# Kernel tuning notes

Measured on AMD Instinct MI355X. Metric: run time of the kernel, lower is better.

## Reference

```python
import jax, jax.numpy as jnp
import numpy as np

D_MODEL = 1024
NUM_HEADS = 16
D_HEAD = D_MODEL // NUM_HEADS
LN_EPS = 1e-5
ROPE_BASE = 10000.0


def layer_norm(x, w, b=None, eps=LN_EPS):
    mu = jnp.mean(x, axis=-1, keepdims=True)
    var = jnp.mean(jnp.square(x - mu), axis=-1, keepdims=True)
    y = (x - mu) * jax.lax.rsqrt(var + eps) * w
    return y + b if b is not None else y


def _rotate_half(x):
    x1, x2 = jnp.split(x, 2, axis=-1)
    return jnp.concatenate([-x2, x1], axis=-1)


def apply_rotary(q, k):
    # q, k: [B, S, H, Dh]
    s, dh = q.shape[1], q.shape[-1]
    inv_freq = 1.0 / (ROPE_BASE ** (jnp.arange(0, dh, 2, dtype=jnp.float32) / dh))
    t = jnp.arange(s, dtype=jnp.float32)
    freqs = jnp.outer(t, inv_freq)                      # [S, Dh/2]
    emb = jnp.concatenate([freqs, freqs], axis=-1)      # [S, Dh]
    cos = jnp.cos(emb)[None, :, None, :].astype(q.dtype)
    sin = jnp.sin(emb)[None, :, None, :].astype(q.dtype)
    q_rot = q * cos + _rotate_half(q) * sin
    k_rot = k * cos + _rotate_half(k) * sin
    return q_rot, k_rot


def setup_inputs() -> dict:
    key = jax.random.key(0)
    ks = jax.random.split(key, 8)
    B, L, D = 4, 2048, D_MODEL
    x = jax.random.normal(ks[0], (B, L, D), dtype=jnp.float32)
    sequence_id = jnp.sort(jax.random.randint(ks[1], (B, L), 0, 8), axis=-1).astype(jnp.int64)
    scale = 1.0 / np.sqrt(D)
    return {
        "x": x,
        "sequence_id": sequence_id,
        "ln_w": jnp.ones((D,), jnp.float32),
        "ln_b": jnp.zeros((D,), jnp.float32),
        "w_qkv": jax.random.normal(ks[2], (D, 3 * D), jnp.float32) * scale,
        "q_ln_w": jnp.ones((D,), jnp.float32),
        "k_ln_w": jnp.ones((D,), jnp.float32),
        "w_out": jax.random.normal(ks[3], (D, D), jnp.float32) * scale,
    }


def reference(x, sequence_id, ln_w, ln_b, w_qkv, q_ln_w, k_ln_w, w_out):
    B, L, D = x.shape
    H, Dh = NUM_HEADS, D_HEAD
    # fused LayerNorm + QKV projection
    qkv = layer_norm(x, ln_w, ln_b) @ w_qkv              # [B, L, 3D]
    q, k, v = jnp.split(qkv, 3, axis=-1)
    # qk layernorm (scale only, bias=False)
    q = layer_norm(q, q_ln_w)
    k = layer_norm(k, k_ln_w)
    # split heads and apply rotary
    q = q.reshape(B, L, H, Dh)
    k = k.reshape(B, L, H, Dh)
    q, k = apply_rotary(q, k)
    v = v.reshape(B, L, H, Dh)
    # packed-sequence mask: tokens attend only within same sequence id
    mask = (sequence_id[:, :, None] == sequence_id[:, None, :])[:, None, :, :]  # [B,1,L,L]
    scale = 1.0 / np.sqrt(Dh)
    scores = jnp.einsum("bqhd,bkhd->bhqk", q, k) * scale
    scores = jnp.where(mask, scores, jnp.finfo(scores.dtype).min)
    attn = jax.nn.softmax(scores, axis=-1)
    ctx = jnp.einsum("bhqk,bkhd->bqhd", attn, v).reshape(B, L, D)
    return ctx @ w_out
```

## Files before the change

kernel.cpp:

```cpp
#include <hip/hip_runtime.h>
#include <hip/hip_bf16.h>
#include <cstdint>
#include <cstddef>
#include <type_traits>

#define D_MODEL 1024
#define NH      16
#define DH      64
#define LSEQ    2048
#define BATCH   4
#define NTOK    8192
#define K3      3072

typedef __attribute__((ext_vector_type(8))) short  short8;
typedef __attribute__((ext_vector_type(4))) float  floatx4;

__device__ __forceinline__ unsigned short f2bf_bits(float f) {
  __hip_bfloat16 h = __float2bfloat16(f);
  return __builtin_bit_cast(unsigned short, h);
}
__device__ __forceinline__ float bf2f(unsigned short u) {
  return __bfloat162float(__builtin_bit_cast(__hip_bfloat16, u));
}
__device__ __forceinline__ unsigned int pack_bf16(float lo, float hi) {
  return (unsigned int)f2bf_bits(lo) | ((unsigned int)f2bf_bits(hi) << 16);
}

__device__ __forceinline__ void gld_lds16(const void* g, void* l) {
  __builtin_amdgcn_global_load_lds(
      (const __attribute__((address_space(1))) void*)g,
      (__attribute__((address_space(3))) void*)l,
      16, 0, 0);
}

__global__ __launch_bounds__(256)
void prep_kernel(const float* __restrict__ x, const float* __restrict__ ln_w,
                 const float* __restrict__ ln_b, const float* __restrict__ w_qkv,
                 const float* __restrict__ w_out, const int* __restrict__ sid,
                 __hip_bfloat16* __restrict__ hbuf, __hip_bfloat16* __restrict__ wqkvT,
                 __hip_bfloat16* __restrict__ woutT, int* __restrict__ segstart,
                 int* __restrict__ segend) {
  __shared__ __align__(16) char smem[8448];
  const int blk = blockIdx.x;
  const int tid = threadIdx.x;

  if (blk < 4096) {
    float (*tile)[33] = reinterpret_cast<float(*)[33]>(smem);
    const float* src;  __hip_bfloat16* dst;  int R, C, bx, by;
    if (blk < 3072) { src = w_qkv; dst = wqkvT; R = 1024; C = 3072; bx = blk % 96; by = blk / 96; }
    else            { src = w_out; dst = woutT; R = 1024; C = 1024; bx = (blk - 3072) & 31; by = (blk - 3072) >> 5; }
    const int c0 = bx * 32, r0 = by * 32;
    const int xx = tid & 31, yy = tid >> 5;
    #pragma unroll
    for (int j = 0; j < 32; j += 8)
      tile[yy + j][xx] = src[(size_t)(r0 + yy + j) * C + c0 + xx];
    __syncthreads();
    #pragma unroll
    for (int j = 0; j < 32; j += 8)
      dst[(size_t)(c0 + yy + j) * R + r0 + xx] = __float2bfloat16(tile[xx][yy + j]);
  } else if (blk < 6144) {
    const int lane = tid & 63;
    const int t = (blk - 4096) * 4 + (tid >> 6);
    const float4* xr = reinterpret_cast<const float4*>(x) + (size_t)t * 256;
    float4 v[4];
    float s = 0.f, ss = 0.f;
    #pragma unroll
    for (int i = 0; i < 4; i++) {
      v[i] = xr[lane + i * 64];
      s  += (v[i].x + v[i].y) + (v[i].z + v[i].w);
      ss += (v[i].x*v[i].x + v[i].y*v[i].y) + (v[i].z*v[i].z + v[i].w*v[i].w);
    }
    #pragma unroll
    for (int off = 1; off < 64; off <<= 1) {
      s  += __shfl_xor(s, off);
      ss += __shfl_xor(ss, off);
    }
    const float mu = s * (1.f / 1024);
    const float rs = rsqrtf(ss * (1.f / 1024) - mu * mu + 1e-5f);
    const float4* wr = reinterpret_cast<const float4*>(ln_w);
    const float4* br = reinterpret_cast<const float4*>(ln_b);
    ushort4* hr = reinterpret_cast<ushort4*>(hbuf) + (size_t)t * 256;
    #pragma unroll
    for (int i = 0; i < 4; i++) {
      const float4 wv = wr[lane + i * 64];
      const float4 bv = br[lane + i * 64];
      ushort4 o;
      o.x = f2bf_bits((v[i].x - mu) * rs * wv.x + bv.x);
      o.y = f2bf_bits((v[i].y - mu) * rs * wv.y + bv.y);
      o.z = f2bf_bits((v[i].z - mu) * rs * wv.z + bv.z);
      o.w = f2bf_bits((v[i].w - mu) * rs * wv.w + bv.w);
      hr[lane + i * 64] = o;
    }
  } else {
    int* srow = reinterpret_cast<int*>(smem);
    const int sblk = blk - 6144;
    const int b = sblk >> 3;
    const int* row = sid + (size_t)b * LSEQ;
    #pragma unroll
    for (int i = 0; i < 8; i++) srow[tid + i * 256] = row[tid + i * 256];
    __syncthreads();
    const int l = (sblk & 7) * 256 + tid;
    const int v = srow[l];
    int lo = 0, hi = l;
    while (lo < hi) { int mid = (lo + hi) >> 1; if (srow[mid] < v) lo = mid + 1; else hi = mid; }
    const int i = b * LSEQ + l;
    segstart[i] = lo;
    lo = l + 1; hi = LSEQ;
    while (lo < hi) { int mid = (lo + hi) >> 1; if (srow[mid] <= v) lo = mid + 1; else hi = mid; }
    segend[i] = lo;
  }
}

template <typename OutT>
__global__ __launch_bounds__(256, 2)
void gemm_bt(const __hip_bfloat16* __restrict__ A, const __hip_bfloat16* __restrict__ Bt,
             OutT* __restrict__ C, int M, int N, int K) {
  const int tid  = threadIdx.x;
  const int lane = tid & 63;
  const int wave = tid >> 6;
  const int bm = blockIdx.y * 128;
  const int bn = blockIdx.x * 128;
  const int wm = (wave & 1) * 64;
  const int wn = (wave >> 1) * 64;
  const int quad = lane >> 4;
  const int l16  = lane & 15;

  __shared__ __align__(16) __hip_bfloat16 As[128 * 64];
  __shared__ __align__(16) __hip_bfloat16 Bs[128 * 64];

  floatx4 acc[4][4];
  #pragma unroll
  for (int i = 0; i < 4; i++)
    #pragma unroll
    for (int j = 0; j < 4; j++) {
      floatx4 z = {0.f, 0.f, 0.f, 0.f};
      acc[i][j] = z;
    }

  const int srow = tid >> 3;
  const int sq   = tid & 7;
  const int sc8  = (sq ^ (srow & 7)) * 8;
  const __hip_bfloat16* Ab = A  + (size_t)(bm + srow) * K + sc8;
  const __hip_bfloat16* Bb = Bt + (size_t)(bn + srow) * K + sc8;

  const int axr = l16 & 7;

  for (int k0 = 0; k0 < K; k0 += 64) {
    __syncthreads();
    #pragma unroll
    for (int p = 0; p < 4; p++) {
      gld_lds16(Ab + (size_t)(p * 32) * K + k0, (char*)As + p * 4096 + tid * 16);
      gld_lds16(Bb + (size_t)(p * 32) * K + k0, (char*)Bs + p * 4096 + tid * 16);
    }
    __syncthreads();
    #pragma unroll
    for (int s0 = 0; s0 < 2; s0++) {
      const int qo = ((s0 * 4 + quad) ^ axr) * 8;
      short8 af[4], bfr[4];
      #pragma unroll
      for (int i = 0; i < 4; i++)
        af[i] = *reinterpret_cast<const short8*>(As + (wm + i * 16 + l16) * 64 + qo);
      #pragma unroll
      for (int j = 0; j < 4; j++)
        bfr[j] = *reinterpret_cast<const short8*>(Bs + (wn + j * 16 + l16) * 64 + qo);
      #pragma unroll
      for (int i = 0; i < 4; i++)
        #pragma unroll
        for (int j = 0; j < 4; j++)
          acc[i][j] = __builtin_amdgcn_mfma_f32_16x16x32_bf16(af[i], bfr[j], acc[i][j], 0, 0, 0);
    }
  }

  #pragma unroll
  for (int i = 0; i < 4; i++)
    #pragma unroll
    for (int j = 0; j < 4; j++) {
      const int row0 = bm + wm + i * 16 + quad * 4;
      const int col  = bn + wn + j * 16 + l16;
      #pragma unroll
      for (int r = 0; r < 4; r++) {
        if constexpr (std::is_same<OutT, __hip_bfloat16>::value)
          C[(size_t)(row0 + r) * N + col] = __float2bfloat16(acc[i][j][r]);
        else
          C[(size_t)(row0 + r) * N + col] = acc[i][j][r];
      }
    }
}

__global__ __launch_bounds__(256)
void ropevt_kernel(const unsigned short* __restrict__ qkv, const float* __restrict__ qw,
                   const float* __restrict__ kw, unsigned short* __restrict__ qT,
                   unsigned short* __restrict__ kT, unsigned short* __restrict__ vT) {
  __shared__ __align__(16) unsigned short T[64 * 64];
  const int blk = blockIdx.x;
  const int tid = threadIdx.x;

  if (blk < 2048) {
    const int lane = tid & 63;
    const int t = blk * 4 + (tid >> 6);
    const int b = t >> 11, l = t & 2047;
    const unsigned short* row = qkv + (size_t)t * K3;
    const int hh = lane >> 2;
    const int jb = (lane & 3) * 8;
    const int base = hh * 64 + jb;

    const short8 qa_u = *reinterpret_cast<const short8*>(row + base);
    const short8 qb_u = *reinterpret_cast<const short8*>(row + base + 32);
    const short8 ka_u = *reinterpret_cast<const short8*>(row + 1024 + base);
    const short8 kb_u = *reinterpret_cast<const short8*>(row + 1024 + base + 32);

    float qa[8], qb[8], ka[8], kb[8];
    float s_q = 0.f, ss_q = 0.f, s_k = 0.f, ss_k = 0.f;
    #pragma unroll
    for (int e = 0; e < 8; e++) {
      qa[e] = bf2f((unsigned short)qa_u[e]); qb[e] = bf2f((unsigned short)qb_u[e]);
      ka[e] = bf2f((unsigned short)ka_u[e]); kb[e] = bf2f((unsigned short)kb_u[e]);
      s_q  += qa[e] + qb[e];  ss_q += qa[e]*qa[e] + qb[e]*qb[e];
      s_k  += ka[e] + kb[e];  ss_k += ka[e]*ka[e] + kb[e]*kb[e];
    }
    #pragma unroll
    for (int off = 1; off < 64; off <<= 1) {
      s_q  += __shfl_xor(s_q, off);  ss_q += __shfl_xor(ss_q, off);
      s_k  += __shfl_xor(s_k, off);  ss_k += __shfl_xor(ss_k, off);
    }
    const float qmu = s_q * (1.f/1024);
    const float qrs = rsqrtf(ss_q * (1.f/1024) - qmu*qmu + 1e-5f);
    const float kmu = s_k * (1.f/1024);
    const float krs = rsqrtf(ss_k * (1.f/1024) - kmu*kmu + 1e-5f);

    const int j0 = lane & 31;
    const float invf = __expf(-(float)j0 * 0.28782313662425575f);
    float tsin, tcos;
    sincosf((float)l * invf, &tsin, &tcos);

    const float4 wq0 = *reinterpret_cast<const float4*>(qw + base);
    const float4 wq1 = *reinterpret_cast<const float4*>(qw + base + 4);
    const float4 wq2 = *reinterpret_cast<const float4*>(qw + base + 32);
    const float4 wq3 = *reinterpret_cast<const float4*>(qw + base + 36);
    const float4 wk0 = *reinterpret_cast<const float4*>(kw + base);
    const float4 wk1 = *reinterpret_cast<const float4*>(kw + base + 4);
    const float4 wk2 = *reinterpret_cast<const float4*>(kw + base + 32);
    const float4 wk3 = *reinterpret_cast<const float4*>(kw + base + 36);
    const float wqa[8] = {wq0.x,wq0.y,wq0.z,wq0.w, wq1.x,wq1.y,wq1.z,wq1.w};
    const float wqb[8] = {wq2.x,wq2.y,wq2.z,wq2.w, wq3.x,wq3.y,wq3.z,wq3.w};
    const float wka[8] = {wk0.x,wk0.y,wk0.z,wk0.w, wk1.x,wk1.y,wk1.z,wk1.w};
    const float wkb[8] = {wk2.x,wk2.y,wk2.z,wk2.w, wk3.x,wk3.y,wk3.z,wk3.w};

    short8 oqa, oqb, oka, okb;
    #pragma unroll
    for (int e = 0; e < 8; e++) {
      const int j = jb + e;
      const float c  = __shfl(tcos, j);
      const float sn = __shfl(tsin, j);
      const float qn1 = (qa[e] - qmu) * qrs * wqa[e];
      const float qn2 = (qb[e] - qmu) * qrs * wqb[e];
      const float kn1 = (ka[e] - kmu) * krs * wka[e];
      const float kn2 = (kb[e] - kmu) * krs * wkb[e];
      oqa[e] = (short)f2bf_bits((qn1 * c - qn2 * sn) * 0.125f);
      oqb[e] = (short)f2bf_bits((qn2 * c + qn1 * sn) * 0.125f);
      oka[e] = (short)f2bf_bits(kn1 * c - kn2 * sn);
      okb[e] = (short)f2bf_bits(kn2 * c + kn1 * sn);
    }
    const size_t ob = ((size_t)(b * NH + hh) * LSEQ + l) * DH + jb;
    *reinterpret_cast<short8*>(qT + ob)      = oqa;
    *reinterpret_cast<short8*>(qT + ob + 32) = oqb;
    *reinterpret_cast<short8*>(kT + ob)      = oka;
    *reinterpret_cast<short8*>(kT + ob + 32) = okb;
  } else {
    const int blkv = blk - 2048;
    const int l0 = (blkv & 31) * 64;
    const int bh = blkv >> 5;
    const int b = bh >> 4, h = bh & 15;
    const int sr = tid >> 3, scc = tid & 7;
    const int r1 = sr + 32;
    gld_lds16(qkv + (size_t)(b * LSEQ + l0 + sr) * K3 + 2048 + h * 64 + ((scc ^ ((sr >> 3) & 7)) * 8),
              (char*)T + tid * 16);
    gld_lds16(qkv + (size_t)(b * LSEQ + l0 + r1) * K3 + 2048 + h * 64 + ((scc ^ ((r1 >> 3) & 7)) * 8),
              (char*)T + 4096 + tid * 16);
    __syncthreads();
    #pragma unroll
    for (int it = 0; it < 2; it++) {
      const int cid = tid + it * 256;
      const int dh = cid >> 3, c = (cid & 7) * 8;
      const int sl = (dh >> 3) ^ ((c >> 3) & 7);
      short8 o;
      #pragma unroll
      for (int e = 0; e < 8; e++)
        o[e] = (short)T[(c + e) * 64 + sl * 8 + (dh & 7)];
      *reinterpret_cast<short8*>(vT + ((size_t)bh * DH + dh) * LSEQ + l0 + c) = o;
    }
  }
}

__global__ __launch_bounds__(256, 2)
void attn_mfma(const unsigned short* __restrict__ qT, const unsigned short* __restrict__ kT,
               const unsigned short* __restrict__ vT, const int* __restrict__ segs,
               const int* __restrict__ sege, unsigned short* __restrict__ ctx) {
  const int tid  = threadIdx.x;
  const int lane = tid & 63, w = tid >> 6;
  const int quad = lane >> 4, l16 = lane & 15;

  const int fid = blockIdx.x + (blockIdx.y << 4) + (blockIdx.z << 8);
  const int sw  = (fid & 7) * 128 + (fid >> 3);
  const int qbase = (sw & 15) * 128;
  const int h = (sw >> 4) & 15, b = sw >> 8;

  const size_t bh = (size_t)(b * NH + h);
  const unsigned short* Kg = kT + bh * LSEQ * DH;
  const unsigned short* Vg = vT + bh * DH * LSEQ;

  __shared__ __align__(16) unsigned short Ps[4][32 * 72];

  short8 qf[2][2];
  int st[2], en[2], gmin[2], gmax[2];
  #pragma unroll
  for (int g = 0; g < 2; g++) {
    const int qy = qbase + w * 32 + g * 16 + l16;
    const unsigned short* Qrow = qT + (bh * LSEQ + qy) * DH;
    qf[g][0] = *reinterpret_cast<const short8*>(Qrow + quad * 8);
    qf[g][1] = *reinterpret_cast<const short8*>(Qrow + 32 + quad * 8);
    st[g] = segs[b * LSEQ + qy];
    en[g] = sege[b * LSEQ + qy];
    gmin[g] = segs[b * LSEQ + qbase + w * 32 + g * 16];
    gmax[g] = sege[b * LSEQ + qbase + w * 32 + g * 16 + 15];
  }
  const int wstart = gmin[0] & ~63;
  const int wmax   = gmax[1];

  floatx4 acc[2][4];
  #pragma unroll
  for (int g = 0; g < 2; g++)
    #pragma unroll
    for (int dt = 0; dt < 4; dt++) { floatx4 z = {0.f,0.f,0.f,0.f}; acc[g][dt] = z; }
  float m[2] = {9.f, 9.f};
  float lsum[2] = {0.f, 0.f};

  short8 kf[4][2];
  #pragma unroll
  for (int t = 0; t < 4; t++) {
    const unsigned short* kp = Kg + (size_t)(wstart + t * 16 + l16) * DH + quad * 8;
    kf[t][0] = *reinterpret_cast<const short8*>(kp);
    kf[t][1] = *reinterpret_cast<const short8*>(kp + 32);
  }

  for (int kk = wstart; kk < wmax; kk += 64) {
    const bool have_next = (kk + 64) < wmax;

    short8 vf[4][2];
    #pragma unroll
    for (int dt = 0; dt < 4; dt++) {
      const unsigned short* vp = Vg + (size_t)(dt * 16 + l16) * LSEQ + kk + quad * 8;
      vf[dt][0] = *reinterpret_cast<const short8*>(vp);
      vf[dt][1] = *reinterpret_cast<const short8*>(vp + 32);
    }
    short8 kn[4][2];
    if (have_next) {
      #pragma unroll
      for (int t = 0; t < 4; t++) {
        const unsigned short* kp = Kg + (size_t)(kk + 64 + t * 16 + l16) * DH + quad * 8;
        kn[t][0] = *reinterpret_cast<const short8*>(kp);
        kn[t][1] = *reinterpret_cast<const short8*>(kp + 32);
      }
    }

    bool act[2];
    #pragma unroll
    for (int g = 0; g < 2; g++)
      act[g] = !(kk + 64 <= gmin[g] || kk >= gmax[g]);

    #pragma unroll
    for (int g = 0; g < 2; g++) {
      if (!act[g]) continue;

      floatx4 sc[4];
      __builtin_amdgcn_s_setprio(1);
      #pragma unroll
      for (int t = 0; t < 4; t++) {
        floatx4 z = {0.f,0.f,0.f,0.f};
        sc[t] = __builtin_amdgcn_mfma_f32_16x16x32_bf16(kf[t][0], qf[g][0], z, 0, 0, 0);
        sc[t] = __builtin_amdgcn_mfma_f32_16x16x32_bf16(kf[t][1], qf[g][1], sc[t], 0, 0, 0);
      }
      __builtin_amdgcn_s_setprio(0);

      const unsigned span = (unsigned)(en[g] - st[g]);
      float vm = -1e30f;
      #pragma unroll
      for (int t = 0; t < 4; t++) {
        const int k0 = kk + t * 16 + quad * 4;
        #pragma unroll
        for (int r = 0; r < 4; r++) {
          const bool ok = (unsigned)(k0 + r - st[g]) < span;
          sc[t][r] = ok ? sc[t][r] : -1e30f;
          vm = fmaxf(vm, sc[t][r]);
        }
      }

      if (__any(vm > m[g])) {
        float vv = fmaxf(vm, __shfl_xor(vm, 16));
        vv = fmaxf(vv, __shfl_xor(vv, 32));
        const float a = __expf(m[g] - vv);
        lsum[g] *= a;
        #pragma unroll
        for (int dt = 0; dt < 4; dt++)
          #pragma unroll
          for (int r = 0; r < 4; r++) acc[g][dt][r] *= a;
        m[g] = vv;
      }

      const float mn = m[g];
      float rs = 0.f;
      #pragma unroll
      for (int t = 0; t < 4; t++) {
        const float p0 = __expf(sc[t][0] - mn);
        const float p1 = __expf(sc[t][1] - mn);
        const float p2 = __expf(sc[t][2] - mn);
        const float p3 = __expf(sc[t][3] - mn);
        rs += (p0 + p1) + (p2 + p3);
        uint2 pk;
        pk.x = pack_bf16(p0, p1);
        pk.y = pack_bf16(p2, p3);
        *reinterpret_cast<uint2*>(&Ps[w][(g * 16 + l16) * 72 + t * 16 + quad * 4]) = pk;
      }
      lsum[g] += rs;
    }

    short8 pf[2][2];
    #pragma unroll
    for (int g = 0; g < 2; g++) {
      if (!act[g]) continue;
      pf[g][0] = *reinterpret_cast<const short8*>(&Ps[w][(g * 16 + l16) * 72 + quad * 8]);
      pf[g][1] = *reinterpret_cast<const short8*>(&Ps[w][(g * 16 + l16) * 72 + 32 + quad * 8]);
    }
    __builtin_amdgcn_s_setprio(1);
    #pragma unroll
    for (int dt = 0; dt < 4; dt++) {
      #pragma unroll
      for (int g = 0; g < 2; g++) {
        if (!act[g]) continue;
        acc[g][dt] = __builtin_amdgcn_mfma_f32_16x16x32_bf16(vf[dt][0], pf[g][0], acc[g][dt], 0, 0, 0);
        acc[g][dt] = __builtin_amdgcn_mfma_f32_16x16x32_bf16(vf[dt][1], pf[g][1], acc[g][dt], 0, 0, 0);
      }
    }
    __builtin_amdgcn_s_setprio(0);

    if (have_next) {
      #pragma unroll
      for (int t = 0; t < 4; t++) {
        kf[t][0] = kn[t][0];
        kf[t][1] = kn[t][1];
      }
    }
  }

  #pragma unroll
  for (int g = 0; g < 2; g++) {
    lsum[g] += __shfl_xor(lsum[g], 16);
    lsum[g] += __shfl_xor(lsum[g], 32);
    const float inv = (lsum[g] > 0.f) ? 1.f / lsum[g] : 0.f;
    const int qy = qbase + w * 32 + g * 16 + l16;
    unsigned short* orow = ctx + ((size_t)(b * LSEQ + qy)) * D_MODEL + h * DH;
    #pragma unroll
    for (int dt = 0; dt < 4; dt++) {
      uint2 o;
      o.x = pack_bf16(acc[g][dt][0] * inv, acc[g][dt][1] * inv);
      o.y = pack_bf16(acc[g][dt][2] * inv, acc[g][dt][3] * inv);
      *reinterpret_cast<uint2*>(orow + dt * 16 + quad * 4) = o;
    }
  }
}

extern "C" void kernel_launch(void* const* d_in, const int* in_sizes, int n_in,
                              void* d_out, int out_size, void* d_ws, size_t ws_size,
                              hipStream_t stream) {
  const float* x      = (const float*)d_in[0];
  const int*   sid    = (const int*)d_in[1];
  const float* ln_w   = (const float*)d_in[2];
  const float* ln_b   = (const float*)d_in[3];
  const float* w_qkv  = (const float*)d_in[4];
  const float* q_ln_w = (const float*)d_in[5];
  const float* k_ln_w = (const float*)d_in[6];
  const float* w_out  = (const float*)d_in[7];
  float* out = (float*)d_out;
  char* ws = (char*)d_ws;

  constexpr size_t OFF_WQKVT = 0;
  constexpr size_t OFF_WOUTT = 6291456;
  constexpr size_t OFF_H     = 8388608;
  constexpr size_t OFF_QKV   = 25165824;
  constexpr size_t OFF_QT    = 75497472;
  constexpr size_t OFF_KT    = 92274688;
  constexpr size_t OFF_VT    = 109051904;
  constexpr size_t OFF_CTX   = 125829120;
  constexpr size_t OFF_SEGS  = 142606336;
  constexpr size_t OFF_SEGE  = 142639104;

  __hip_bfloat16* wqkvT = (__hip_bfloat16*)(ws + OFF_WQKVT);
  __hip_bfloat16* woutT = (__hip_bfloat16*)(ws + OFF_WOUTT);
  __hip_bfloat16* hbuf  = (__hip_bfloat16*)(ws + OFF_H);
  __hip_bfloat16* qkvb  = (__hip_bfloat16*)(ws + OFF_QKV);
  unsigned short* qTb   = (unsigned short*)(ws + OFF_QT);
  unsigned short* kTb   = (unsigned short*)(ws + OFF_KT);
  unsigned short* vTb   = (unsigned short*)(ws + OFF_VT);
  unsigned short* ctx   = (unsigned short*)(ws + OFF_CTX);
  int*            segst = (int*)(ws + OFF_SEGS);
  int*            segen = (int*)(ws + OFF_SEGE);

  prep_kernel<<<6176, 256, 0, stream>>>(x, ln_w, ln_b, w_qkv, w_out, sid,
                                        hbuf, wqkvT, woutT, segst, segen);
  gemm_bt<__hip_bfloat16><<<dim3(K3 / 128, NTOK / 128), 256, 0, stream>>>(
      hbuf, wqkvT, qkvb, NTOK, K3, 1024);
  ropevt_kernel<<<4096, 256, 0, stream>>>((const unsigned short*)qkvb, q_ln_w, k_ln_w,
                                          qTb, kTb, vTb);
  attn_mfma<<<dim3(LSEQ / 128, NH, BATCH), 256, 0, stream>>>(qTb, kTb, vTb, segst, segen, ctx);
  gemm_bt<float><<<dim3(D_MODEL / 128, NTOK / 128), 256, 0, stream>>>(
      (const __hip_bfloat16*)ctx, woutT, out, NTOK, D_MODEL, 1024);
}
```

Before: 254.6 us.

## Split attention key range across wave pairs and merge partial softmax in LDS

The attention kernel now launches 512 threads per block. Each pair of waves shares the same 32 queries and splits the key blocks between them by alternating 64-key chunks. The two partial results (accumulators, running max and sum) are merged through shared memory using a flash-decoding style rescale. This is meant to shorten each wave's serial key loop and raise parallelism, since the packed-sequence mask gives only a few key blocks per query. In exchange it adds an extra LDS buffer, a block-wide barrier, and merge arithmetic, and it drops the block-index swizzle.

```diff
diff --git a/kernel.cpp b/kernel.cpp
--- a/kernel.cpp
+++ b/kernel.cpp
@@ -292,39 +292,40 @@
   }
 }
 
-__global__ __launch_bounds__(256, 2)
+__global__ __launch_bounds__(512, 4)
 void attn_mfma(const unsigned short* __restrict__ qT, const unsigned short* __restrict__ kT,
                const unsigned short* __restrict__ vT, const int* __restrict__ segs,
                const int* __restrict__ sege, unsigned short* __restrict__ ctx) {
   const int tid  = threadIdx.x;
   const int lane = tid & 63, w = tid >> 6;
+  const int pair = w >> 1, half = w & 1;
   const int quad = lane >> 4, l16 = lane & 15;
 
-  const int fid = blockIdx.x + (blockIdx.y << 4) + (blockIdx.z << 8);
-  const int sw  = (fid & 7) * 128 + (fid >> 3);
-  const int qbase = (sw & 15) * 128;
-  const int h = (sw >> 4) & 15, b = sw >> 8;
-
+  const int qbase = blockIdx.x * 128;
+  const int h = blockIdx.y, b = blockIdx.z;
   const size_t bh = (size_t)(b * NH + h);
   const unsigned short* Kg = kT + bh * LSEQ * DH;
   const unsigned short* Vg = vT + bh * DH * LSEQ;
 
-  __shared__ __align__(16) unsigned short Ps[4][32 * 72];
+  __shared__ __align__(16) unsigned short Ps[8][32 * 72];
+  __shared__ __align__(16) float MB[4 * 64 * 37];
+
+  const int qg = qbase + pair * 32;
 
   short8 qf[2][2];
   int st[2], en[2], gmin[2], gmax[2];
   #pragma unroll
   for (int g = 0; g < 2; g++) {
-    const int qy = qbase + w * 32 + g * 16 + l16;
+    const int qy = qg + g * 16 + l16;
     const unsigned short* Qrow = qT + (bh * LSEQ + qy) * DH;
     qf[g][0] = *reinterpret_cast<const short8*>(Qrow + quad * 8);
     qf[g][1] = *reinterpret_cast<const short8*>(Qrow + 32 + quad * 8);
     st[g] = segs[b * LSEQ + qy];
     en[g] = sege[b * LSEQ + qy];
-    gmin[g] = segs[b * LSEQ + qbase + w * 32 + g * 16];
-    gmax[g] = sege[b * LSEQ + qbase + w * 32 + g * 16 + 15];
-  }
-  const int wstart = gmin[0] & ~63;
+    gmin[g] = segs[b * LSEQ + qg + g * 16];
+    gmax[g] = sege[b * LSEQ + qg + g * 16 + 15];
+  }
+  const int wstart = (gmin[0] & ~63) + half * 64;
   const int wmax   = gmax[1];
 
   floatx4 acc[2][4];
@@ -343,8 +344,8 @@
     kf[t][1] = *reinterpret_cast<const short8*>(kp + 32);
   }
 
-  for (int kk = wstart; kk < wmax; kk += 64) {
-    const bool have_next = (kk + 64) < wmax;
+  for (int kk = wstart; kk < wmax; kk += 128) {
+    const bool have_next = (kk + 128) < wmax;
 
     short8 vf[4][2];
     #pragma unroll
@@ -357,7 +358,7 @@
     if (have_next) {
       #pragma unroll
       for (int t = 0; t < 4; t++) {
-        const unsigned short* kp = Kg + (size_t)(kk + 64 + t * 16 + l16) * DH + quad * 8;
+        const unsigned short* kp = Kg + (size_t)(kk + 128 + t * 16 + l16) * DH + quad * 8;
         kn[t][0] = *reinterpret_cast<const short8*>(kp);
         kn[t][1] = *reinterpret_cast<const short8*>(kp + 32);
       }
@@ -456,15 +457,45 @@
   for (int g = 0; g < 2; g++) {
     lsum[g] += __shfl_xor(lsum[g], 16);
     lsum[g] += __shfl_xor(lsum[g], 32);
-    const float inv = (lsum[g] > 0.f) ? 1.f / lsum[g] : 0.f;
-    const int qy = qbase + w * 32 + g * 16 + l16;
-    unsigned short* orow = ctx + ((size_t)(b * LSEQ + qy)) * D_MODEL + h * DH;
-    #pragma unroll
-    for (int dt = 0; dt < 4; dt++) {
-      uint2 o;
-      o.x = pack_bf16(acc[g][dt][0] * inv, acc[g][dt][1] * inv);
-      o.y = pack_bf16(acc[g][dt][2] * inv, acc[g][dt][3] * inv);
-      *reinterpret_cast<uint2*>(orow + dt * 16 + quad * 4) = o;
+  }
+
+  float* mb = MB + ((size_t)(pair * 64 + lane)) * 37;
+  if (half) {
+    #pragma unroll
+    for (int g = 0; g < 2; g++)
+      #pragma unroll
+      for (int dt = 0; dt < 4; dt++)
+        #pragma unroll
+        for (int r = 0; r < 4; r++)
+          mb[g * 16 + dt * 4 + r] = acc[g][dt][r];
+    mb[32] = m[0];  mb[33] = m[1];
+    mb[34] = lsum[0]; mb[35] = lsum[1];
+  }
+  __syncthreads();
+  if (!half) {
+    #pragma unroll
+    for (int g = 0; g < 2; g++) {
+      const float Mo = mb[32 + g];
+      const float Lo = mb[34 + g];
+      const float Mm = fmaxf(m[g], Mo);
+      const float we = __expf(m[g] - Mm);
+      const float wo = __expf(Mo - Mm);
+      const float L  = lsum[g] * we + Lo * wo;
+      const float inv = (L > 0.f) ? 1.f / L : 0.f;
+      const float fe = we * inv, fo = wo * inv;
+      const int qy = qg + g * 16 + l16;
+      unsigned short* orow = ctx + ((size_t)(b * LSEQ + qy)) * D_MODEL + h * DH;
+      #pragma unroll
+      for (int dt = 0; dt < 4; dt++) {
+        const float o0 = acc[g][dt][0] * fe + mb[g * 16 + dt * 4 + 0] * fo;
+        const float o1 = acc[g][dt][1] * fe + mb[g * 16 + dt * 4 + 1] * fo;
+        const float o2 = acc[g][dt][2] * fe + mb[g * 16 + dt * 4 + 2] * fo;
+        const float o3 = acc[g][dt][3] * fe + mb[g * 16 + dt * 4 + 3] * fo;
+        uint2 o;
+        o.x = pack_bf16(o0, o1);
+        o.y = pack_bf16(o2, o3);
+        *reinterpret_cast<uint2*>(orow + dt * 16 + quad * 4) = o;
+      }
     }
   }
 }
@@ -511,7 +542,7 @@
       hbuf, wqkvT, qkvb, NTOK, K3, 1024);
   ropevt_kernel<<<4096, 256, 0, stream>>>((const unsigned short*)qkvb, q_ln_w, k_ln_w,
                                           qTb, kTb, vTb);
-  attn_mfma<<<dim3(LSEQ / 128, NH, BATCH), 256, 0, stream>>>(qTb, kTb, vTb, segst, segen, ctx);
+  attn_mfma<<<dim3(LSEQ / 128, NH, BATCH), 512, 0, stream>>>(qTb, kTb, vTb, segst, segen, ctx);
   gemm_bt<float><<<dim3(D_MODEL / 128, NTOK / 128), 256, 0, stream>>>(
       (const __hip_bfloat16*)ctx, woutT, out, NTOK, D_MODEL, 1024);
 }
```

Result: slower. 369.6 us (+45.2%).
